# Optimization experiments

Hardware: AMD Instinct MI355X
Metric: run time of the kernel (lower is better)

Reference implementation:

```python
import jax, jax.numpy as jnp
import numpy as np

DIM = 1024
NUM_HEADS = 16
HEAD_DIM = 64
EPS = 1e-6

def setup_inputs() -> dict:
    key = jax.random.key(0)
    ks = jax.random.split(key, 6)
    x = jax.random.normal(ks[0], (4, 2048, DIM), dtype=jnp.float32)
    # Linear weights stored as (in, out); torch nn.Linear computes x @ W.T with W (out,in),
    # equivalent math with our (in,out) layout.
    Wq = jax.random.normal(ks[1], (DIM, NUM_HEADS * HEAD_DIM), dtype=jnp.float32) / np.sqrt(DIM)
    Wk = jax.random.normal(ks[2], (DIM, NUM_HEADS * HEAD_DIM), dtype=jnp.float32) / np.sqrt(DIM)
    Wv = jax.random.normal(ks[3], (DIM, NUM_HEADS * HEAD_DIM), dtype=jnp.float32) / np.sqrt(DIM)
    Wo = jax.random.normal(ks[4], (NUM_HEADS * HEAD_DIM, DIM), dtype=jnp.float32) / np.sqrt(NUM_HEADS * HEAD_DIM)
    # FeatureMap buffer: randn(head_dim, head_dim)/sqrt(head_dim)
    proj = jax.random.normal(ks[5], (HEAD_DIM, HEAD_DIM), dtype=jnp.float32) / np.sqrt(HEAD_DIM)
    return {"x": x, "Wq": Wq, "Wk": Wk, "Wv": Wv, "Wo": Wo, "proj": proj}

def _feature_map(x, proj):
    # phi(x) = elu(x @ proj) + 1  (positive features)
    return jax.nn.elu(x @ proj) + 1.0

def reference(x, Wq, Wk, Wv, Wo, proj):
    B, S, _ = x.shape
    H, D = NUM_HEADS, HEAD_DIM
    q = (x @ Wq).reshape(B, S, H, D)
    k = (x @ Wk).reshape(B, S, H, D)
    v = (x @ Wv).reshape(B, S, H, D)
    q = _feature_map(q, proj)
    k = _feature_map(k, proj)
    # scan over time: carry kv_state (B,H,D,D) and k_state (B,H,D)
    q_t = jnp.moveaxis(q, 1, 0)  # (S,B,H,D)
    k_t = jnp.moveaxis(k, 1, 0)
    v_t = jnp.moveaxis(v, 1, 0)

    def step(carry, qkv):
        kv, ksum = carry
        qt, kt, vt = qkv  # each (B,H,D)
        kv = kv + kt[..., :, None] * vt[..., None, :]  # outer product k v^T
        ksum = ksum + kt
        num = jnp.einsum('bhd,bhde->bhe', qt, kv)
        den = jnp.einsum('bhd,bhd->bh', qt, ksum) + EPS
        return (kv, ksum), num / den[..., None]

    kv0 = jnp.zeros((B, H, D, D), dtype=x.dtype)
    ks0 = jnp.zeros((B, H, D), dtype=x.dtype)
    _, out = jax.lax.scan(step, (kv0, ks0), (q_t, k_t, v_t))
    out = jnp.moveaxis(out, 0, 1).reshape(B, S, H * D)  # (B,S,H*D)
    return out @ Wo
```

## Files before the change

### kernel.cpp

```cpp
#include <hip/hip_runtime.h>

typedef unsigned short u16;
typedef unsigned int   u32;
typedef short bfrag8 __attribute__((ext_vector_type(8)));
typedef float facc4  __attribute__((ext_vector_type(4)));

#define DIM    1024
#define NH     16
#define HD     64
#define BSZ    4
#define SEQ    2048
#define MROWS  (BSZ*SEQ)
#define CHUNK  64
#define NCHUNK (SEQ/CHUNK)
#define BH     (BSZ*NH)
#define TS     72
#define NT     16

__device__ __forceinline__ u16 f2bf(float f) {
  u32 u = __builtin_bit_cast(u32, f);
  u32 r = u + 0x7fffu + ((u >> 16) & 1u);
  return (u16)(r >> 16);
}
__device__ __forceinline__ float bf2f(u16 b) {
  return __builtin_bit_cast(float, (u32)b << 16);
}

__device__ __forceinline__ void gload_lds16(const void* g, void* l) {
  __builtin_amdgcn_global_load_lds((const __attribute__((address_space(1))) u32*)g,
                                   (__attribute__((address_space(3))) u32*)l, 16, 0, 0);
}

__global__ __launch_bounds__(256) void prep(const float* __restrict__ x,
                                            const float* __restrict__ Wq, const float* __restrict__ Wk,
                                            const float* __restrict__ Wv, const float* __restrict__ Wo,
                                            const float* __restrict__ proj,
                                            u16* __restrict__ xb, u16* __restrict__ wt) {
  __shared__ float smem[6144];
  const int bx = blockIdx.x, tid = threadIdx.x;
  if (bx < 8192) {
    const int i = (bx * 256 + tid) * 4;
    const float4 v = *(const float4*)(x + i);
    ushort4 o;
    o.x = f2bf(v.x); o.y = f2bf(v.y); o.z = f2bf(v.z); o.w = f2bf(v.w);
    *(ushort4*)(xb + i) = o;
  } else if (bx < 9216) {
    const int idx = bx - 8192;
    const int i0 = (idx & 31) * 32;
    const int h  = (idx >> 5) & 15;
    const int sel = idx >> 9;
    const float* W = sel ? Wk : Wq;
    u16* out = wt + (size_t)sel * (DIM*DIM);
    float* sp = smem;
    float* sw = smem + 4096;
    for (int s = tid; s < 4096; s += 256) sp[s] = proj[s];
    for (int s = tid; s < 2048; s += 256) {
      int r = s >> 6, c = s & 63;
      sw[s] = W[(size_t)(i0 + r)*DIM + h*64 + c];
    }
    __syncthreads();
    const int i  = tid >> 3;
    const int e0 = (tid & 7) * 8;
    #pragma unroll
    for (int ee = 0; ee < 8; ++ee) {
      const int e = e0 + ee;
      float acc = 0.f;
      for (int d = 0; d < 64; ++d) acc += sw[i*64 + d] * sp[d*64 + e];
      out[(size_t)(h*64 + e)*DIM + i0 + i] = f2bf(acc);
    }
  } else {
    const int idx = bx - 9216;
    const int n0 = (idx & 31) * 32;
    const int k0 = ((idx >> 5) & 31) * 32;
    const int sel = idx >> 10;
    const float* in = sel ? Wo : Wv;
    u16* out = wt + (size_t)(2 + sel) * (DIM*DIM);
    float* tile = smem;
    for (int s = tid; s < 1024; s += 256) {
      int r = s >> 5, c = s & 31;
      tile[r*33 + c] = in[(size_t)(k0 + r)*DIM + n0 + c];
    }
    __syncthreads();
    for (int s = tid; s < 1024; s += 256) {
      int r = s >> 5, c = s & 31;
      out[(size_t)(n0 + r)*DIM + k0 + c] = f2bf(tile[c*33 + r]);
    }
  }
}

#define SBAR0() __builtin_amdgcn_sched_barrier(0)

#define STAGE6(kt, bp) { \
  const int rih = tid >> 3, sl = tid & 7; \
  const int gc = ((sl ^ (rih & 7)) << 3); \
  _Pragma("unroll") for (int seg = 0; seg < 2; ++seg) \
    gload_lds16(A + (size_t)(m0 + seg*64 + rih)*DIM + (kt)*64 + gc, (bp) + seg*4096 + tid*8); \
  _Pragma("unroll") for (int seg = 0; seg < 4; ++seg) \
    gload_lds16(W + (size_t)(ngl + seg*64 + rih)*DIM + (kt)*64 + gc, (bp) + 8192 + seg*4096 + tid*8); \
}

#define RD8(xd, wd, bp, KH) { \
  _Pragma("unroll") for (int mf = 0; mf < 4; ++mf) { \
    const int row = wm*64 + mf*16 + lr; \
    xd[mf] = *(const bfrag8*)&(bp)[row*64 + ((((KH)*4+g) ^ (row & 7)) << 3)]; } \
  _Pragma("unroll") for (int nf = 0; nf < 4; ++nf) { \
    const int row = wn*64 + nf*16 + lr; \
    wd[nf] = *(const bfrag8*)&(bp)[8192 + row*64 + ((((KH)*4+g) ^ (row & 7)) << 3)]; } \
}

#define MM16(xs, ws) { __builtin_amdgcn_s_setprio(1); \
  _Pragma("unroll") for (int nf = 0; nf < 4; ++nf) \
    _Pragma("unroll") for (int mf = 0; mf < 4; ++mf) \
      acc[nf][mf] = __builtin_amdgcn_mfma_f32_16x16x32_bf16(ws[nf], xs[mf], acc[nf][mf], 0, 0, 0); \
  __builtin_amdgcn_s_setprio(0); }

template<int MODE>
__global__ __launch_bounds__(512, 1)
void gemmK(const u16* __restrict__ A, const u16* __restrict__ W,
           u16* __restrict__ outb, float* __restrict__ outf) {
  __shared__ u16 lds[2*24576];
  const int tid  = threadIdx.x;
  const int wave = tid >> 6, lane = tid & 63;
  const int wm = wave >> 2, wn = wave & 3;
  const int lr = lane & 15, g = lane >> 4;

  const int NY  = (MODE == 0) ? 12 : 4;
  const int q   = (int)gridDim.x >> 3;
  const int bid = (int)blockIdx.x;
  const int nf_ = (bid & 7) * q + (bid >> 3);
  const int m0  = (nf_ / NY) * 128;
  const int ngl = (nf_ % NY) * 256;

  STAGE6(0, lds);
  STAGE6(1, lds + 24576);
  asm volatile("s_waitcnt vmcnt(6)" ::: "memory");
  asm volatile("s_barrier" ::: "memory");

  facc4 acc[4][4] = {};
  bfrag8 xa[4], wa[4], xb[4], wb[4];

  RD8(xa, wa, lds, 0);

  #pragma unroll 2
  for (int t = 0; t < NT; ++t) {
    u16* bufp = lds + (t & 1) * 24576;
    u16* bufq = lds + ((t + 1) & 1) * 24576;
    asm volatile("s_waitcnt lgkmcnt(0)" ::: "memory"); SBAR0();
    RD8(xb, wb, bufp, 1);
    SBAR0();
    MM16(xa, wa);
    SBAR0();
    asm volatile("s_waitcnt vmcnt(0)" ::: "memory");
    asm volatile("s_barrier" ::: "memory");
    asm volatile("s_waitcnt lgkmcnt(0)" ::: "memory"); SBAR0();
    if (t + 2 < NT) STAGE6(t + 2, bufp);
    if (t + 1 < NT) RD8(xa, wa, bufq, 0);
    SBAR0();
    MM16(xb, wb);
    SBAR0();
    asm volatile("s_barrier" ::: "memory");
  }

  const int sel = (MODE == 0) ? (ngl >> 10) : 0;
  const bool doElu = (MODE == 0) && (sel < 2);
  const int coly = (MODE == 0) ? (ngl & 1023) : ngl;
  #pragma unroll
  for (int nf = 0; nf < 4; ++nf) {
    #pragma unroll
    for (int mf = 0; mf < 4; ++mf) {
      const facc4 a = acc[nf][mf];
      const int m = m0 + wm*64 + mf*16 + lr;
      const int col0 = coly + wn*64 + nf*16 + g*4;
      float v0 = a[0], v1 = a[1], v2 = a[2], v3 = a[3];
      if (MODE == 0) {
        if (doElu) {
          v0 = (v0 > 0.f) ? (v0 + 1.f) : __expf(v0);
          v1 = (v1 > 0.f) ? (v1 + 1.f) : __expf(v1);
          v2 = (v2 > 0.f) ? (v2 + 1.f) : __expf(v2);
          v3 = (v3 > 0.f) ? (v3 + 1.f) : __expf(v3);
        }
        uint2 pk;
        pk.x = (u32)f2bf(v0) | ((u32)f2bf(v1) << 16);
        pk.y = (u32)f2bf(v2) | ((u32)f2bf(v3) << 16);
        *(uint2*)&outb[(size_t)sel*((size_t)MROWS*DIM) + (size_t)m*DIM + col0] = pk;
      } else {
        float4 pk; pk.x = v0; pk.y = v1; pk.z = v2; pk.w = v3;
        *(float4*)&outf[(size_t)m*DIM + col0] = pk;
      }
    }
  }
}


__global__ __launch_bounds__(256) void phaseA(const u16* __restrict__ Kb, const u16* __restrict__ Vb,
                                              u16* __restrict__ Ast, float* __restrict__ ksum) {
  const int c = blockIdx.x, bh = blockIdx.y;
  const int b = bh >> 4, h = bh & 15;
  const int tid = threadIdx.x;
  const int wave = tid >> 6, lane = tid & 63, lr = lane & 15, g = lane >> 4;
  __shared__ u16 lKt[64*TS];
  __shared__ u16 lVt[64*TS];
  const size_t mbase = (size_t)b*SEQ + (size_t)c*CHUNK;

  for (int s = tid; s < 512; s += 256) {
    const int t = s >> 3, dg = (s & 7) * 8;
    const bfrag8 kk = *(const bfrag8*)&Kb[(mbase + t)*DIM + h*64 + dg];
    const bfrag8 vv = *(const bfrag8*)&Vb[(mbase + t)*DIM + h*64 + dg];
    #pragma unroll
    for (int j = 0; j < 8; ++j) {
      lKt[(dg + j)*TS + t] = (u16)kk[j];
      lVt[(dg + j)*TS + t] = (u16)vv[j];
    }
  }
  __syncthreads();

  facc4 acc[4] = {};
  #pragma unroll
  for (int kt = 0; kt < 2; ++kt) {
    const bfrag8 af = *(const bfrag8*)&lVt[(wave*16 + lr)*TS + kt*32 + g*8];
    #pragma unroll
    for (int j = 0; j < 4; ++j) {
      const bfrag8 bk = *(const bfrag8*)&lKt[(j*16 + lr)*TS + kt*32 + g*8];
      acc[j] = __builtin_amdgcn_mfma_f32_16x16x32_bf16(af, bk, acc[j], 0, 0, 0);
    }
  }
  u16* dst = Ast + (((size_t)bh*NCHUNK + c) << 12);
  #pragma unroll
  for (int j = 0; j < 4; ++j)
    #pragma unroll
    for (int r = 0; r < 4; ++r)
      dst[(wave*16 + g*4 + r)*64 + j*16 + lr] = f2bf(acc[j][r]);

  const int d = tid >> 2, seg = tid & 3;
  const bfrag8 k0 = *(const bfrag8*)&lKt[d*TS + seg*16];
  const bfrag8 k1 = *(const bfrag8*)&lKt[d*TS + seg*16 + 8];
  float s = 0.f;
  #pragma unroll
  for (int j = 0; j < 8; ++j) s += bf2f((u16)k0[j]) + bf2f((u16)k1[j]);
  s += __shfl_xor(s, 1, 64);
  s += __shfl_xor(s, 2, 64);
  if (seg == 0) ksum[((size_t)bh*NCHUNK + c)*64 + d] = s;
}

__global__ __launch_bounds__(256) void phaseC(const u16* __restrict__ Qb, const u16* __restrict__ Kb,
                                              const u16* __restrict__ Vb, const u16* __restrict__ Ast,
                                              const float* __restrict__ ksum, u16* __restrict__ Ob) {
  const int c = blockIdx.x, bh = blockIdx.y;
  const int b = bh >> 4, h = bh & 15;
  const int tid = threadIdx.x;
  const int wave = tid >> 6, lane = tid & 63, lr = lane & 15, g = lane >> 4;
  __shared__ u16 lS  [64*TS];
  __shared__ u16 lVt [64*TS];
  __shared__ u16 lKVt[64*TS];
  __shared__ float lks[64];
  __shared__ float lrs[64];
  __shared__ float lqk[64];
  const size_t mbase = (size_t)b*SEQ + (size_t)c*CHUNK;

  for (int s = tid; s < 512; s += 256) {
    const int t = s >> 3, dg = (s & 7) * 8;
    const bfrag8 vv = *(const bfrag8*)&Vb[(mbase + t)*DIM + h*64 + dg];
    #pragma unroll
    for (int j = 0; j < 8; ++j) lVt[(dg + j)*TS + t] = (u16)vv[j];
  }
  {
    float pacc[16] = {};
    const u16* abase = Ast + (((size_t)bh*NCHUNK) << 12) + tid*16;
    for (int cc = 0; cc < c; ++cc) {
      const bfrag8 a0 = *(const bfrag8*)&abase[(size_t)cc*4096];
      const bfrag8 a1 = *(const bfrag8*)&abase[(size_t)cc*4096 + 8];
      #pragma unroll
      for (int jj = 0; jj < 8; ++jj) {
        pacc[jj]     += bf2f((u16)a0[jj]);
        pacc[8 + jj] += bf2f((u16)a1[jj]);
      }
    }
    const int e = tid >> 2, d0 = (tid & 3) * 16;
    #pragma unroll
    for (int jj = 0; jj < 16; ++jj) lKVt[e*TS + d0 + jj] = f2bf(pacc[jj]);
  }
  if (tid < 64) {
    float s = 0.f;
    const float* kb = ksum + (size_t)bh*NCHUNK*64 + tid;
    for (int cc = 0; cc < c; ++cc) s += kb[(size_t)cc*64];
    lks[tid] = s;
  }

  bfrag8 qf[2], kf[4][2];
  {
    const u16* qrow = Qb + (mbase + wave*16 + lr)*DIM + h*64;
    qf[0] = *(const bfrag8*)&qrow[g*8];
    qf[1] = *(const bfrag8*)&qrow[32 + g*8];
  }
  #pragma unroll
  for (int j = 0; j < 4; ++j) {
    const u16* krow = Kb + (mbase + j*16 + lr)*DIM + h*64;
    kf[j][0] = *(const bfrag8*)&krow[g*8];
    kf[j][1] = *(const bfrag8*)&krow[32 + g*8];
  }

  facc4 accs[4] = {};
  #pragma unroll
  for (int kt = 0; kt < 2; ++kt)
    #pragma unroll
    for (int j = 0; j < 4; ++j)
      accs[j] = __builtin_amdgcn_mfma_f32_16x16x32_bf16(qf[kt], kf[j][kt], accs[j], 0, 0, 0);

  float rs[4] = {0.f, 0.f, 0.f, 0.f};
  #pragma unroll
  for (int j = 0; j < 4; ++j) {
    const int cc = j*16 + lr;
    #pragma unroll
    for (int r = 0; r < 4; ++r) {
      const int rr = wave*16 + g*4 + r;
      const float vS = (cc <= rr) ? accs[j][r] : 0.f;
      rs[r] += vS;
      lS[rr*TS + cc] = f2bf(vS);
    }
  }
  #pragma unroll
  for (int r = 0; r < 4; ++r) {
    float t = rs[r];
    t += __shfl_xor(t, 1, 64); t += __shfl_xor(t, 2, 64);
    t += __shfl_xor(t, 4, 64); t += __shfl_xor(t, 8, 64);
    if (lr == 0) lrs[wave*16 + g*4 + r] = t;
  }
  __syncthreads();

  {
    const u16* qr2 = Qb + (mbase + wave*16 + lr)*DIM + h*64 + g*16;
    const bfrag8 a0 = *(const bfrag8*)&qr2[0];
    const bfrag8 a1 = *(const bfrag8*)&qr2[8];
    float t = 0.f;
    #pragma unroll
    for (int j = 0; j < 8; ++j)
      t += bf2f((u16)a0[j]) * lks[g*16 + j] + bf2f((u16)a1[j]) * lks[g*16 + 8 + j];
    t += __shfl_xor(t, 16, 64);
    t += __shfl_xor(t, 32, 64);
    if (g == 0) lqk[wave*16 + lr] = t;
  }

  facc4 acco[4] = {};
  #pragma unroll
  for (int kt = 0; kt < 2; ++kt) {
    const bfrag8 sf = *(const bfrag8*)&lS[(wave*16 + lr)*TS + kt*32 + g*8];
    #pragma unroll
    for (int j = 0; j < 4; ++j) {
      const bfrag8 vf = *(const bfrag8*)&lVt[(j*16 + lr)*TS + kt*32 + g*8];
      acco[j] = __builtin_amdgcn_mfma_f32_16x16x32_bf16(sf, vf, acco[j], 0, 0, 0);
    }
  }
  #pragma unroll
  for (int kt = 0; kt < 2; ++kt)
    #pragma unroll
    for (int j = 0; j < 4; ++j) {
      const bfrag8 kvf = *(const bfrag8*)&lKVt[(j*16 + lr)*TS + kt*32 + g*8];
      acco[j] = __builtin_amdgcn_mfma_f32_16x16x32_bf16(qf[kt], kvf, acco[j], 0, 0, 0);
    }

  #pragma unroll
  for (int r = 0; r < 4; ++r) {
    const int rr = wave*16 + g*4 + r;
    const float rden = 1.0f / (lrs[rr] + lqk[rr] + 1e-6f);
    #pragma unroll
    for (int j = 0; j < 4; ++j)
      Ob[(mbase + rr)*DIM + h*64 + j*16 + lr] = f2bf(acco[j][r] * rden);
  }
}

extern "C" void kernel_launch(void* const* d_in, const int* in_sizes, int n_in,
                              void* d_out, int out_size, void* d_ws, size_t ws_size,
                              hipStream_t stream) {
  const float* x    = (const float*)d_in[0];
  const float* Wq   = (const float*)d_in[1];
  const float* Wk   = (const float*)d_in[2];
  const float* Wv   = (const float*)d_in[3];
  const float* Wo   = (const float*)d_in[4];
  const float* proj = (const float*)d_in[5];
  float* out = (float*)d_out;

  char* ws = (char*)d_ws;
  u16*   xb   = (u16*)  (ws);
  u16*   wt   = (u16*)  (ws + 16777216);
  u16*   qkv  = (u16*)  (ws + 25165824);
  u16*   Ob   = (u16*)  (ws + 75497472);
  u16*   Ast  = (u16*)  (ws + 92274688);
  float* ksum = (float*)(ws + 109051904);
  (void)ws_size; (void)in_sizes; (void)n_in; (void)out_size;

  prep<<<dim3(11264), 256, 0, stream>>>(x, Wq, Wk, Wv, Wo, proj, xb, wt);

  gemmK<0><<<dim3(64*12), 512, 0, stream>>>(xb, wt, qkv, nullptr);

  const u16* Qb = qkv;
  const u16* Kb = qkv + (size_t)MROWS*DIM;
  const u16* Vb = qkv + 2*(size_t)MROWS*DIM;

  phaseA<<<dim3(NCHUNK, BH), 256, 0, stream>>>(Kb, Vb, Ast, ksum);
  phaseC<<<dim3(NCHUNK, BH), 256, 0, stream>>>(Qb, Kb, Vb, Ast, ksum, Ob);

  gemmK<1><<<dim3(64*4), 512, 0, stream>>>(Ob, wt + 3*(size_t)DIM*DIM, nullptr, out);
}
```

Measured before the change: 213.0 us.

## Add separate exclusive prefix-scan kernel for chunk KV states

Adds a phaseB kernel that does an exclusive prefix sum over chunks of the per-chunk KV outer-product states and key sums, in place. phaseC then loads one precomputed prefix state instead of re-summing every earlier chunk, which turns quadratic redundant reads of Ast into linear work. The cost is one extra kernel launch and a serial 32-step scan per element. Each running sum is rounded to bf16 on store, which may change numerics slightly.

```diff
diff --git a/kernel.cpp b/kernel.cpp
--- a/kernel.cpp
+++ b/kernel.cpp
@@ -242,6 +242,23 @@
   if (seg == 0) ksum[((size_t)bh*NCHUNK + c)*64 + d] = s;
 }
 
+__global__ __launch_bounds__(256) void phaseB(u16* __restrict__ Ast, float* __restrict__ ksum) {
+  const int bh = blockIdx.x, slice = blockIdx.y;
+  const int tid = threadIdx.x;
+  u16* base = Ast + (size_t)bh*NCHUNK*4096 + slice*256 + tid;
+  float v[NCHUNK];
+  #pragma unroll
+  for (int c = 0; c < NCHUNK; ++c) v[c] = bf2f(base[(size_t)c*4096]);
+  float run = 0.f;
+  #pragma unroll
+  for (int c = 0; c < NCHUNK; ++c) { base[(size_t)c*4096] = f2bf(run); run += v[c]; }
+  if (slice == 0 && tid < 64) {
+    float rs = 0.f;
+    float* kp = ksum + (size_t)bh*NCHUNK*64 + tid;
+    for (int c = 0; c < NCHUNK; ++c) { const float t = kp[c*64]; kp[c*64] = rs; rs += t; }
+  }
+}
+
 __global__ __launch_bounds__(256) void phaseC(const u16* __restrict__ Qb, const u16* __restrict__ Kb,
                                               const u16* __restrict__ Vb, const u16* __restrict__ Ast,
                                               const float* __restrict__ ksum, u16* __restrict__ Ob) {
@@ -263,28 +280,12 @@
     #pragma unroll
     for (int j = 0; j < 8; ++j) lVt[(dg + j)*TS + t] = (u16)vv[j];
   }
-  {
-    float pacc[16] = {};
-    const u16* abase = Ast + (((size_t)bh*NCHUNK) << 12) + tid*16;
-    for (int cc = 0; cc < c; ++cc) {
-      const bfrag8 a0 = *(const bfrag8*)&abase[(size_t)cc*4096];
-      const bfrag8 a1 = *(const bfrag8*)&abase[(size_t)cc*4096 + 8];
-      #pragma unroll
-      for (int jj = 0; jj < 8; ++jj) {
-        pacc[jj]     += bf2f((u16)a0[jj]);
-        pacc[8 + jj] += bf2f((u16)a1[jj]);
-      }
-    }
-    const int e = tid >> 2, d0 = (tid & 3) * 16;
-    #pragma unroll
-    for (int jj = 0; jj < 16; ++jj) lKVt[e*TS + d0 + jj] = f2bf(pacc[jj]);
-  }
-  if (tid < 64) {
-    float s = 0.f;
-    const float* kb = ksum + (size_t)bh*NCHUNK*64 + tid;
-    for (int cc = 0; cc < c; ++cc) s += kb[(size_t)cc*64];
-    lks[tid] = s;
-  }
+  const u16* kvsrc = Ast + (((size_t)bh*NCHUNK + c) << 12);
+  for (int s = tid; s < 512; s += 256) {
+    const int e = s >> 3, dg = (s & 7) * 8;
+    *(bfrag8*)&lKVt[e*TS + dg] = *(const bfrag8*)&kvsrc[e*64 + dg];
+  }
+  if (tid < 64) lks[tid] = ksum[((size_t)bh*NCHUNK + c)*64 + tid];
 
   bfrag8 qf[2], kf[4][2];
   {
@@ -397,6 +398,7 @@
   const u16* Vb = qkv + 2*(size_t)MROWS*DIM;
 
   phaseA<<<dim3(NCHUNK, BH), 256, 0, stream>>>(Kb, Vb, Ast, ksum);
+  phaseB<<<dim3(BH, 16), 256, 0, stream>>>(Ast, ksum);
   phaseC<<<dim3(NCHUNK, BH), 256, 0, stream>>>(Qb, Kb, Vb, Ast, ksum, Ob);
 
   gemmK<1><<<dim3(64*4), 512, 0, stream>>>(Ob, wt + 3*(size_t)DIM*DIM, nullptr, out);
```

Result: faster. 188.5 us (-11.5%).

## Fuse chunked linear-attention phases into a single sequential scan kernel

Applied to the files above, without the earlier changes.

Replaces the two-kernel chunk scheme with one kernel per (batch, head, 16-column slice of V). The old scheme stored per-chunk KV outer products to global memory, and each chunk later re-summed all earlier ones, which is quadratic in the number of chunks. The new kernel walks the chunks in order and keeps the running KV state in MFMA accumulators and the running k-sum in shared memory. It also prefetches the next chunk's Q/K/V into registers while the current chunk is computed. The cost is a serial loop of 32 chunks per block with only 256 blocks, and the QK^T product is recomputed by each of the 4 column-slice blocks.

```diff
diff --git a/kernel.cpp b/kernel.cpp
--- a/kernel.cpp
+++ b/kernel.cpp
@@ -191,180 +191,152 @@
   }
 }
 
-
-__global__ __launch_bounds__(256) void phaseA(const u16* __restrict__ Kb, const u16* __restrict__ Vb,
-                                              u16* __restrict__ Ast, float* __restrict__ ksum) {
-  const int c = blockIdx.x, bh = blockIdx.y;
+__global__ __launch_bounds__(256) void scanF(const u16* __restrict__ Qb, const u16* __restrict__ Kb,
+                                             const u16* __restrict__ Vb, u16* __restrict__ Ob) {
+  const int bx = blockIdx.x;
+  const int bh = bx & 63, eq = bx >> 6;
   const int b = bh >> 4, h = bh & 15;
   const int tid = threadIdx.x;
   const int wave = tid >> 6, lane = tid & 63, lr = lane & 15, g = lane >> 4;
+
+  __shared__ u16 lQ [64*TS];
+  __shared__ u16 lK [64*TS];
   __shared__ u16 lKt[64*TS];
-  __shared__ u16 lVt[64*TS];
-  const size_t mbase = (size_t)b*SEQ + (size_t)c*CHUNK;
-
-  for (int s = tid; s < 512; s += 256) {
-    const int t = s >> 3, dg = (s & 7) * 8;
-    const bfrag8 kk = *(const bfrag8*)&Kb[(mbase + t)*DIM + h*64 + dg];
-    const bfrag8 vv = *(const bfrag8*)&Vb[(mbase + t)*DIM + h*64 + dg];
-    #pragma unroll
-    for (int j = 0; j < 8; ++j) {
-      lKt[(dg + j)*TS + t] = (u16)kk[j];
-      lVt[(dg + j)*TS + t] = (u16)vv[j];
-    }
-  }
-  __syncthreads();
-
-  facc4 acc[4] = {};
-  #pragma unroll
-  for (int kt = 0; kt < 2; ++kt) {
-    const bfrag8 af = *(const bfrag8*)&lVt[(wave*16 + lr)*TS + kt*32 + g*8];
-    #pragma unroll
-    for (int j = 0; j < 4; ++j) {
-      const bfrag8 bk = *(const bfrag8*)&lKt[(j*16 + lr)*TS + kt*32 + g*8];
-      acc[j] = __builtin_amdgcn_mfma_f32_16x16x32_bf16(af, bk, acc[j], 0, 0, 0);
-    }
-  }
-  u16* dst = Ast + (((size_t)bh*NCHUNK + c) << 12);
-  #pragma unroll
-  for (int j = 0; j < 4; ++j)
-    #pragma unroll
-    for (int r = 0; r < 4; ++r)
-      dst[(wave*16 + g*4 + r)*64 + j*16 + lr] = f2bf(acc[j][r]);
-
-  const int d = tid >> 2, seg = tid & 3;
-  const bfrag8 k0 = *(const bfrag8*)&lKt[d*TS + seg*16];
-  const bfrag8 k1 = *(const bfrag8*)&lKt[d*TS + seg*16 + 8];
-  float s = 0.f;
-  #pragma unroll
-  for (int j = 0; j < 8; ++j) s += bf2f((u16)k0[j]) + bf2f((u16)k1[j]);
-  s += __shfl_xor(s, 1, 64);
-  s += __shfl_xor(s, 2, 64);
-  if (seg == 0) ksum[((size_t)bh*NCHUNK + c)*64 + d] = s;
-}
-
-__global__ __launch_bounds__(256) void phaseC(const u16* __restrict__ Qb, const u16* __restrict__ Kb,
-                                              const u16* __restrict__ Vb, const u16* __restrict__ Ast,
-                                              const float* __restrict__ ksum, u16* __restrict__ Ob) {
-  const int c = blockIdx.x, bh = blockIdx.y;
-  const int b = bh >> 4, h = bh & 15;
-  const int tid = threadIdx.x;
-  const int wave = tid >> 6, lane = tid & 63, lr = lane & 15, g = lane >> 4;
-  __shared__ u16 lS  [64*TS];
-  __shared__ u16 lVt [64*TS];
-  __shared__ u16 lKVt[64*TS];
+  __shared__ u16 lVt[16*TS];
+  __shared__ u16 lS [64*TS];
+  __shared__ u16 lKV[16*TS];
   __shared__ float lks[64];
   __shared__ float lrs[64];
   __shared__ float lqk[64];
-  const size_t mbase = (size_t)b*SEQ + (size_t)c*CHUNK;
-
-  for (int s = tid; s < 512; s += 256) {
-    const int t = s >> 3, dg = (s & 7) * 8;
-    const bfrag8 vv = *(const bfrag8*)&Vb[(mbase + t)*DIM + h*64 + dg];
-    #pragma unroll
-    for (int j = 0; j < 8; ++j) lVt[(dg + j)*TS + t] = (u16)vv[j];
-  }
+
+  if (tid < 64) lks[tid] = 0.f;
+  facc4 akv = {};
+
+  bfrag8 qr[2], kr[2], vr;
   {
-    float pacc[16] = {};
-    const u16* abase = Ast + (((size_t)bh*NCHUNK) << 12) + tid*16;
-    for (int cc = 0; cc < c; ++cc) {
-      const bfrag8 a0 = *(const bfrag8*)&abase[(size_t)cc*4096];
-      const bfrag8 a1 = *(const bfrag8*)&abase[(size_t)cc*4096 + 8];
-      #pragma unroll
-      for (int jj = 0; jj < 8; ++jj) {
-        pacc[jj]     += bf2f((u16)a0[jj]);
-        pacc[8 + jj] += bf2f((u16)a1[jj]);
-      }
-    }
-    const int e = tid >> 2, d0 = (tid & 3) * 16;
-    #pragma unroll
-    for (int jj = 0; jj < 16; ++jj) lKVt[e*TS + d0 + jj] = f2bf(pacc[jj]);
-  }
-  if (tid < 64) {
-    float s = 0.f;
-    const float* kb = ksum + (size_t)bh*NCHUNK*64 + tid;
-    for (int cc = 0; cc < c; ++cc) s += kb[(size_t)cc*64];
-    lks[tid] = s;
-  }
-
-  bfrag8 qf[2], kf[4][2];
-  {
-    const u16* qrow = Qb + (mbase + wave*16 + lr)*DIM + h*64;
-    qf[0] = *(const bfrag8*)&qrow[g*8];
-    qf[1] = *(const bfrag8*)&qrow[32 + g*8];
-  }
-  #pragma unroll
-  for (int j = 0; j < 4; ++j) {
-    const u16* krow = Kb + (mbase + j*16 + lr)*DIM + h*64;
-    kf[j][0] = *(const bfrag8*)&krow[g*8];
-    kf[j][1] = *(const bfrag8*)&krow[32 + g*8];
-  }
-
-  facc4 accs[4] = {};
-  #pragma unroll
-  for (int kt = 0; kt < 2; ++kt)
-    #pragma unroll
-    for (int j = 0; j < 4; ++j)
-      accs[j] = __builtin_amdgcn_mfma_f32_16x16x32_bf16(qf[kt], kf[j][kt], accs[j], 0, 0, 0);
-
-  float rs[4] = {0.f, 0.f, 0.f, 0.f};
-  #pragma unroll
-  for (int j = 0; j < 4; ++j) {
-    const int cc = j*16 + lr;
+    const size_t mb = (size_t)b*SEQ;
+    #pragma unroll
+    for (int i = 0; i < 2; ++i) {
+      const int s = i*256 + tid, t = s >> 3, dg = (s & 7)*8;
+      qr[i] = *(const bfrag8*)&Qb[(mb + t)*DIM + h*64 + dg];
+      kr[i] = *(const bfrag8*)&Kb[(mb + t)*DIM + h*64 + dg];
+    }
+    if (tid < 128) {
+      const int t = tid >> 1, dg = (tid & 1)*8;
+      vr = *(const bfrag8*)&Vb[(mb + t)*DIM + h*64 + eq*16 + dg];
+    }
+  }
+  __syncthreads();
+
+  for (int c = 0; c < NCHUNK; ++c) {
+    const size_t mbase = (size_t)b*SEQ + (size_t)c*CHUNK;
+    #pragma unroll
+    for (int i = 0; i < 2; ++i) {
+      const int s = i*256 + tid, t = s >> 3, dg = (s & 7)*8;
+      *(bfrag8*)&lQ[t*TS + dg] = qr[i];
+      *(bfrag8*)&lK[t*TS + dg] = kr[i];
+      #pragma unroll
+      for (int j = 0; j < 8; ++j) lKt[(dg + j)*TS + t] = (u16)kr[i][j];
+    }
+    if (tid < 128) {
+      const int t = tid >> 1, dg = (tid & 1)*8;
+      #pragma unroll
+      for (int j = 0; j < 8; ++j) lVt[(dg + j)*TS + t] = (u16)vr[j];
+    }
+    #pragma unroll
+    for (int r = 0; r < 4; ++r) lKV[(g*4 + r)*TS + wave*16 + lr] = f2bf(akv[r]);
+    __syncthreads();
+
+    if (c + 1 < NCHUNK) {
+      const size_t mb = (size_t)b*SEQ + (size_t)(c + 1)*CHUNK;
+      #pragma unroll
+      for (int i = 0; i < 2; ++i) {
+        const int s = i*256 + tid, t = s >> 3, dg = (s & 7)*8;
+        qr[i] = *(const bfrag8*)&Qb[(mb + t)*DIM + h*64 + dg];
+        kr[i] = *(const bfrag8*)&Kb[(mb + t)*DIM + h*64 + dg];
+      }
+      if (tid < 128) {
+        const int t = tid >> 1, dg = (tid & 1)*8;
+        vr = *(const bfrag8*)&Vb[(mb + t)*DIM + h*64 + eq*16 + dg];
+      }
+    }
+
+    bfrag8 qf[2];
+    qf[0] = *(const bfrag8*)&lQ[(wave*16 + lr)*TS + g*8];
+    qf[1] = *(const bfrag8*)&lQ[(wave*16 + lr)*TS + 32 + g*8];
+    facc4 accs[4] = {};
+    #pragma unroll
+    for (int kt = 0; kt < 2; ++kt)
+      #pragma unroll
+      for (int j = 0; j < 4; ++j) {
+        const bfrag8 kfj = *(const bfrag8*)&lK[(j*16 + lr)*TS + kt*32 + g*8];
+        accs[j] = __builtin_amdgcn_mfma_f32_16x16x32_bf16(qf[kt], kfj, accs[j], 0, 0, 0);
+      }
+    float rs[4] = {0.f, 0.f, 0.f, 0.f};
+    #pragma unroll
+    for (int j = 0; j < 4; ++j) {
+      const int cc = j*16 + lr;
+      #pragma unroll
+      for (int r = 0; r < 4; ++r) {
+        const int rr = wave*16 + g*4 + r;
+        const float vS = (cc <= rr) ? accs[j][r] : 0.f;
+        rs[r] += vS;
+        lS[rr*TS + cc] = f2bf(vS);
+      }
+    }
+    #pragma unroll
+    for (int r = 0; r < 4; ++r) {
+      float tt = rs[r];
+      tt += __shfl_xor(tt, 1, 64); tt += __shfl_xor(tt, 2, 64);
+      tt += __shfl_xor(tt, 4, 64); tt += __shfl_xor(tt, 8, 64);
+      if (lr == 0) lrs[wave*16 + g*4 + r] = tt;
+    }
+    {
+      float tt = 0.f;
+      #pragma unroll
+      for (int j = 0; j < 8; ++j)
+        tt += bf2f((u16)qf[0][j]) * lks[g*8 + j] + bf2f((u16)qf[1][j]) * lks[32 + g*8 + j];
+      tt += __shfl_xor(tt, 16, 64);
+      tt += __shfl_xor(tt, 32, 64);
+      if (g == 0) lqk[wave*16 + lr] = tt;
+    }
+    facc4 acco = {};
+    bfrag8 vf[2];
+    #pragma unroll
+    for (int kt = 0; kt < 2; ++kt) {
+      const bfrag8 sf = *(const bfrag8*)&lS[(wave*16 + lr)*TS + kt*32 + g*8];
+      vf[kt] = *(const bfrag8*)&lVt[lr*TS + kt*32 + g*8];
+      acco = __builtin_amdgcn_mfma_f32_16x16x32_bf16(sf, vf[kt], acco, 0, 0, 0);
+    }
+    #pragma unroll
+    for (int kt = 0; kt < 2; ++kt) {
+      const bfrag8 kvf = *(const bfrag8*)&lKV[lr*TS + kt*32 + g*8];
+      acco = __builtin_amdgcn_mfma_f32_16x16x32_bf16(qf[kt], kvf, acco, 0, 0, 0);
+    }
+    #pragma unroll
+    for (int kt = 0; kt < 2; ++kt) {
+      const bfrag8 bk = *(const bfrag8*)&lKt[(wave*16 + lr)*TS + kt*32 + g*8];
+      akv = __builtin_amdgcn_mfma_f32_16x16x32_bf16(vf[kt], bk, akv, 0, 0, 0);
+    }
     #pragma unroll
     for (int r = 0; r < 4; ++r) {
       const int rr = wave*16 + g*4 + r;
-      const float vS = (cc <= rr) ? accs[j][r] : 0.f;
-      rs[r] += vS;
-      lS[rr*TS + cc] = f2bf(vS);
-    }
-  }
-  #pragma unroll
-  for (int r = 0; r < 4; ++r) {
-    float t = rs[r];
-    t += __shfl_xor(t, 1, 64); t += __shfl_xor(t, 2, 64);
-    t += __shfl_xor(t, 4, 64); t += __shfl_xor(t, 8, 64);
-    if (lr == 0) lrs[wave*16 + g*4 + r] = t;
-  }
-  __syncthreads();
-
-  {
-    const u16* qr2 = Qb + (mbase + wave*16 + lr)*DIM + h*64 + g*16;
-    const bfrag8 a0 = *(const bfrag8*)&qr2[0];
-    const bfrag8 a1 = *(const bfrag8*)&qr2[8];
-    float t = 0.f;
-    #pragma unroll
-    for (int j = 0; j < 8; ++j)
-      t += bf2f((u16)a0[j]) * lks[g*16 + j] + bf2f((u16)a1[j]) * lks[g*16 + 8 + j];
-    t += __shfl_xor(t, 16, 64);
-    t += __shfl_xor(t, 32, 64);
-    if (g == 0) lqk[wave*16 + lr] = t;
-  }
-
-  facc4 acco[4] = {};
-  #pragma unroll
-  for (int kt = 0; kt < 2; ++kt) {
-    const bfrag8 sf = *(const bfrag8*)&lS[(wave*16 + lr)*TS + kt*32 + g*8];
-    #pragma unroll
-    for (int j = 0; j < 4; ++j) {
-      const bfrag8 vf = *(const bfrag8*)&lVt[(j*16 + lr)*TS + kt*32 + g*8];
-      acco[j] = __builtin_amdgcn_mfma_f32_16x16x32_bf16(sf, vf, acco[j], 0, 0, 0);
-    }
-  }
-  #pragma unroll
-  for (int kt = 0; kt < 2; ++kt)
-    #pragma unroll
-    for (int j = 0; j < 4; ++j) {
-      const bfrag8 kvf = *(const bfrag8*)&lKVt[(j*16 + lr)*TS + kt*32 + g*8];
-      acco[j] = __builtin_amdgcn_mfma_f32_16x16x32_bf16(qf[kt], kvf, acco[j], 0, 0, 0);
-    }
-
-  #pragma unroll
-  for (int r = 0; r < 4; ++r) {
-    const int rr = wave*16 + g*4 + r;
-    const float rden = 1.0f / (lrs[rr] + lqk[rr] + 1e-6f);
-    #pragma unroll
-    for (int j = 0; j < 4; ++j)
-      Ob[(mbase + rr)*DIM + h*64 + j*16 + lr] = f2bf(acco[j][r] * rden);
+      const float rden = 1.0f / (lrs[rr] + lqk[rr] + 1e-6f);
+      Ob[(mbase + rr)*DIM + h*64 + eq*16 + lr] = f2bf(acco[r] * rden);
+    }
+    __syncthreads();
+    {
+      const int d = tid >> 2, seg = tid & 3;
+      const bfrag8 k0 = *(const bfrag8*)&lKt[d*TS + seg*16];
+      const bfrag8 k1 = *(const bfrag8*)&lKt[d*TS + seg*16 + 8];
+      float s = 0.f;
+      #pragma unroll
+      for (int j = 0; j < 8; ++j) s += bf2f((u16)k0[j]) + bf2f((u16)k1[j]);
+      s += __shfl_xor(s, 1, 64);
+      s += __shfl_xor(s, 2, 64);
+      if (seg == 0) lks[d] += s;
+    }
+    __syncthreads();
   }
 }
 
@@ -384,8 +356,6 @@
   u16*   wt   = (u16*)  (ws + 16777216);
   u16*   qkv  = (u16*)  (ws + 25165824);
   u16*   Ob   = (u16*)  (ws + 75497472);
-  u16*   Ast  = (u16*)  (ws + 92274688);
-  float* ksum = (float*)(ws + 109051904);
   (void)ws_size; (void)in_sizes; (void)n_in; (void)out_size;
 
   prep<<<dim3(11264), 256, 0, stream>>>(x, Wq, Wk, Wv, Wo, proj, xb, wt);
@@ -396,8 +366,7 @@
   const u16* Kb = qkv + (size_t)MROWS*DIM;
   const u16* Vb = qkv + 2*(size_t)MROWS*DIM;
 
-  phaseA<<<dim3(NCHUNK, BH), 256, 0, stream>>>(Kb, Vb, Ast, ksum);
-  phaseC<<<dim3(NCHUNK, BH), 256, 0, stream>>>(Qb, Kb, Vb, Ast, ksum, Ob);
+  scanF<<<dim3(256), 256, 0, stream>>>(Qb, Kb, Vb, Ob);
 
   gemmK<1><<<dim3(64*4), 512, 0, stream>>>(Ob, wt + 3*(size_t)DIM*DIM, nullptr, out);
 }
```

New measurement: 222.7 us. +4.6%, slower.
